# Kernel optimization log

Measured on AMD Instinct MI355X. Metric: run time of the kernel, lower is better.

## Reference

```python
import jax, jax.numpy as jnp
import numpy as np
from jax import lax

B, T, I, H = 8192, 512, 3, 25  # batch, seq_len, input_size, hidden_size


def setup_inputs() -> dict:
    key = jax.random.key(0)
    ks = jax.random.split(key, 4)
    x = jax.random.normal(ks[0], (B, T, I), dtype=jnp.float32)
    # xavier-uniform-ish scale for w_ih, orthogonal-ish (plain normal here) for w_hh
    w_ih = jax.random.normal(ks[1], (4 * H, I), dtype=jnp.float32) * 0.5
    w_hh = jax.random.normal(ks[2], (4 * H, H), dtype=jnp.float32) * 0.2
    b_ih = jnp.zeros((4 * H,), dtype=jnp.float32)
    # PyTorch init in module: forget-gate bias (second quarter) set to 1 on each bias
    b_ih = b_ih.at[H:2 * H].set(1.0)
    b_hh = jnp.zeros((4 * H,), dtype=jnp.float32)
    b_hh = b_hh.at[H:2 * H].set(1.0)
    w_lin = jax.random.normal(ks[3], (1, H), dtype=jnp.float32) * 0.3
    b_lin = jnp.zeros((1,), dtype=jnp.float32)
    return {"x": x, "w_ih": w_ih, "w_hh": w_hh, "b_ih": b_ih, "b_hh": b_hh,
            "w_lin": w_lin, "b_lin": b_lin}


def _lstm_last_h(x, w_ih, w_hh, b_ih, b_hh):
    # x: [B, T, I]; returns final hidden state h_T: [B, H]
    b = b_ih + b_hh  # [4H]
    xT = jnp.swapaxes(x, 0, 1)  # [T, B, I]

    def step(carry, x_t):
        h, c = carry
        gates = x_t @ w_ih.T + h @ w_hh.T + b  # [B, 4H]
        i, f, g, o = jnp.split(gates, 4, axis=-1)  # PyTorch gate order i,f,g,o
        i = jax.nn.sigmoid(i)
        f = jax.nn.sigmoid(f)
        g = jnp.tanh(g)
        o = jax.nn.sigmoid(o)
        c = f * c + i * g
        h = o * jnp.tanh(c)
        return (h, c), None

    h0 = jnp.zeros((x.shape[0], w_hh.shape[1]), dtype=x.dtype)
    (h, _), _ = lax.scan(step, (h0, h0), xT)
    return h


def reference(x, w_ih, w_hh, b_ih, b_hh, w_lin, b_lin):
    h_last = _lstm_last_h(x, w_ih, w_hh, b_ih, b_hh)  # [B, H]
    return h_last @ w_lin.T + b_lin  # [B, 1]
```

## Files before the change

kernel.cpp:

```cpp
#include <hip/hip_runtime.h>
#include <hip/hip_bf16.h>


#define TSTEPS 512
#define ISZ 3
#define HSZ 25
#define NW 7
#define CHUNK 256
#define TSTRIDE 40

typedef __attribute__((ext_vector_type(8))) short bf16x8;
typedef __attribute__((ext_vector_type(4))) float f32x4;

__device__ __forceinline__ unsigned short bf16_bits(float v) {
    return __builtin_bit_cast(unsigned short, __float2bfloat16(v));
}
__device__ __forceinline__ unsigned int pack_bf16(float lo, float hi) {
    return ((unsigned int)bf16_bits(hi) << 16) | (unsigned int)bf16_bits(lo);
}

__device__ __forceinline__ void lstm_act(const f32x4 acc, float& c, float& h) {
    const float K1 = 1.442695040888963f;
    const float K2 = 2.885390081777927f;
    const float e0 = __builtin_amdgcn_exp2f(-K1 * acc[0]);
    const float e1 = __builtin_amdgcn_exp2f(-K1 * acc[1]);
    const float e2 = __builtin_amdgcn_exp2f(fminf(-K2 * acc[2], 126.0f));
    const float e3 = __builtin_amdgcn_exp2f(-K1 * acc[3]);
    const float f  = __builtin_amdgcn_rcpf(1.0f + e1);
    const float ig = (1.0f - e2) * __builtin_amdgcn_rcpf((1.0f + e0) * (1.0f + e2));
    c = fmaf(f, c, ig);
    const float ec = __builtin_amdgcn_exp2f(fminf(-K2 * c, 126.0f));
    h = (1.0f - ec) * __builtin_amdgcn_rcpf((1.0f + e3) * (1.0f + ec));
}

__global__ __launch_bounds__(NW * 64) void lstm_mfma(
    const float* __restrict__ x,
    const float* __restrict__ w_ih,
    const float* __restrict__ w_hh,
    const float* __restrict__ b_ih,
    const float* __restrict__ b_hh,
    const float* __restrict__ w_lin,
    const float* __restrict__ b_lin,
    float* __restrict__ out)
{
    __shared__ uint2 xpk[2][CHUNK][16];
    __shared__ short hb[2][2][16 * TSTRIDE];
    __shared__ float outred[2][NW][16];

    const int tid  = threadIdx.x;
    const int w    = tid >> 6;
    const int lane = tid & 63;
    const int n    = lane & 15;
    const int q    = lane >> 4;
    const bool isq0 = (q == 0);
    const int u    = 4 * w + q;
    const bool act = (w < 6) || isq0;

    for (int i = tid; i < 2 * 2 * 16 * TSTRIDE; i += NW * 64) ((short*)hb)[i] = 0;

    auto stage = [&](int c0) {
        const int bsel = tid & 31;
        const int tile = bsel >> 4, nn = bsel & 15;
        const float* __restrict__ g =
            x + (size_t)(blockIdx.x * 32 + bsel) * (TSTEPS * ISZ) + c0 * ISZ;
        for (int tg = tid >> 5; tg < CHUNK / 4; tg += 14) {
            const float4* f4 = (const float4*)(g + tg * 12);
            float4 a = f4[0], b4 = f4[1], c4 = f4[2];
            const float s[4][3] = { {a.x, a.y, a.z}, {a.w, b4.x, b4.y},
                                    {b4.z, b4.w, c4.x}, {c4.y, c4.z, c4.w} };
            #pragma unroll
            for (int uu = 0; uu < 4; ++uu) {
                uint2 d;
                d.x = pack_bf16(s[uu][0], s[uu][1]);
                d.y = pack_bf16(s[uu][2], 1.0f);
                xpk[tile][tg * 4 + uu][nn] = d;
            }
        }
    };
    stage(0);

    bf16x8 afrag;
    #pragma unroll
    for (int j = 0; j < 8; ++j) {
        const int k = q * 8 + j;
        const int r = 16 * w + n;
        const int uu = r >> 2, g = r & 3;
        float v = 0.0f;
        if (uu < HSZ) {
            const int orow = g * HSZ + uu;
            if (k < ISZ)            v = w_ih[orow * ISZ + k];
            else if (k == ISZ)      v = b_ih[orow] + b_hh[orow];
            else if (k < 4 + HSZ)   v = w_hh[orow * HSZ + (k - 4)];
        }
        afrag[j] = (short)bf16_bits(v);
    }

    __syncthreads();

    float cA = 0.f, hA = 0.f, cB = 0.f, hB = 0.f;

    #pragma unroll 1
    for (int t = 0; t < TSTEPS; ++t) {
        if (t == CHUNK) {
            stage(CHUNK);
            __syncthreads();
        }
        const int ts = t & (CHUNK - 1);
        const uint2 xA = xpk[0][ts][n];
        const uint2 xB = xpk[1][ts][n];
        bf16x8 bfA = *reinterpret_cast<const bf16x8*>(&hb[t & 1][0][n * TSTRIDE + q * 8]);
        bf16x8 bfB = *reinterpret_cast<const bf16x8*>(&hb[t & 1][1][n * TSTRIDE + q * 8]);

        uint4 biA = __builtin_bit_cast(uint4, bfA);
        uint4 biB = __builtin_bit_cast(uint4, bfB);
        if (isq0) {
            biA.x = xA.x; biA.y = xA.y;
            biB.x = xB.x; biB.y = xB.y;
        }
        const f32x4 accA = __builtin_amdgcn_mfma_f32_16x16x32_bf16(
            afrag, __builtin_bit_cast(bf16x8, biA),
            (f32x4){0.f, 0.f, 0.f, 0.f}, 0, 0, 0);
        const f32x4 accB = __builtin_amdgcn_mfma_f32_16x16x32_bf16(
            afrag, __builtin_bit_cast(bf16x8, biB),
            (f32x4){0.f, 0.f, 0.f, 0.f}, 0, 0, 0);

        lstm_act(accA, cA, hA);
        lstm_act(accB, cB, hB);

        if (act) {
            hb[(t + 1) & 1][0][n * TSTRIDE + 4 + u] = (short)bf16_bits(hA);
            hb[(t + 1) & 1][1][n * TSTRIDE + 4 + u] = (short)bf16_bits(hB);
        }
        __syncthreads();
    }

    float vA = 0.f, vB = 0.f;
    if (act) { vA = w_lin[u] * hA; vB = w_lin[u] * hB; }
    vA += __shfl_xor(vA, 16); vA += __shfl_xor(vA, 32);
    vB += __shfl_xor(vB, 16); vB += __shfl_xor(vB, 32);
    if (lane < 16) { outred[0][w][lane] = vA; outred[1][w][lane] = vB; }
    __syncthreads();
    if (tid < 32) {
        const int tile = tid >> 4, nn = tid & 15;
        float s = b_lin[0];
        #pragma unroll
        for (int k = 0; k < NW; ++k) s += outred[tile][k][nn];
        out[blockIdx.x * 32 + tile * 16 + nn] = s;
    }
}

extern "C" void kernel_launch(void* const* d_in, const int* in_sizes, int n_in,
                              void* d_out, int out_size, void* d_ws, size_t ws_size,
                              hipStream_t stream) {
    const float* x     = (const float*)d_in[0];
    const float* w_ih  = (const float*)d_in[1];
    const float* w_hh  = (const float*)d_in[2];
    const float* b_ih  = (const float*)d_in[3];
    const float* b_hh  = (const float*)d_in[4];
    const float* w_lin = (const float*)d_in[5];
    const float* b_lin = (const float*)d_in[6];
    float* out = (float*)d_out;

    lstm_mfma<<<8192 / 32, NW * 64, 0, stream>>>(x, w_ih, w_hh, b_ih, b_hh,
                                                 w_lin, b_lin, out);
}
```

Baseline: 317.2 us.

## Shrink block to four waves, each computing two gate fragments per step

The block drops from seven waves to four. Each of the first three waves now computes two 16-row weight fragments per timestep (four MFMAs plus four activations), and the last wave handles the remaining fragment. The aim is to cut per-step barrier cost and increase work per wave, so the latency-bound recurrence spends less time synchronising. In exchange each wave's serial chain per step gets longer, the waves are imbalanced, and register use rises.

New measurement: 348.6 us. +9.9%, slower.

```diff
diff --git a/kernel.cpp b/kernel.cpp
--- a/kernel.cpp
+++ b/kernel.cpp
@@ -5,7 +5,7 @@
 #define TSTEPS 512
 #define ISZ 3
 #define HSZ 25
-#define NW 7
+#define NW 4
 #define CHUNK 256
 #define TSTRIDE 40
 
@@ -53,8 +53,13 @@
     const int n    = lane & 15;
     const int q    = lane >> 4;
     const bool isq0 = (q == 0);
-    const int u    = 4 * w + q;
-    const bool act = (w < 6) || isq0;
+
+    const int f0 = (w < 3) ? 2 * w : 6;
+    const int f1 = (w < 3) ? 2 * w + 1 : 6;
+    const bool use1 = (w < 3);
+    const int u0 = 4 * f0 + q;
+    const int u1 = 4 * f1 + q;
+    const bool m0 = (u0 < HSZ);
 
     for (int i = tid; i < 2 * 2 * 16 * TSTRIDE; i += NW * 64) ((short*)hb)[i] = 0;
 
@@ -63,7 +68,7 @@
         const int tile = bsel >> 4, nn = bsel & 15;
         const float* __restrict__ g =
             x + (size_t)(blockIdx.x * 32 + bsel) * (TSTEPS * ISZ) + c0 * ISZ;
-        for (int tg = tid >> 5; tg < CHUNK / 4; tg += 14) {
+        for (int tg = tid >> 5; tg < CHUNK / 4; tg += (NW * 64) / 32) {
             const float4* f4 = (const float4*)(g + tg * 12);
             float4 a = f4[0], b4 = f4[1], c4 = f4[2];
             const float s[4][3] = { {a.x, a.y, a.z}, {a.w, b4.x, b4.y},
@@ -79,25 +84,32 @@
     };
     stage(0);
 
-    bf16x8 afrag;
+    bf16x8 af0, af1;
     #pragma unroll
-    for (int j = 0; j < 8; ++j) {
-        const int k = q * 8 + j;
-        const int r = 16 * w + n;
-        const int uu = r >> 2, g = r & 3;
-        float v = 0.0f;
-        if (uu < HSZ) {
-            const int orow = g * HSZ + uu;
-            if (k < ISZ)            v = w_ih[orow * ISZ + k];
-            else if (k == ISZ)      v = b_ih[orow] + b_hh[orow];
-            else if (k < 4 + HSZ)   v = w_hh[orow * HSZ + (k - 4)];
-        }
-        afrag[j] = (short)bf16_bits(v);
+    for (int idx = 0; idx < 2; ++idx) {
+        const int T = idx ? f1 : f0;
+        bf16x8 af;
+        #pragma unroll
+        for (int j = 0; j < 8; ++j) {
+            const int k = q * 8 + j;
+            const int r = 16 * T + n;
+            const int uu = r >> 2, g = r & 3;
+            float v = 0.0f;
+            if (uu < HSZ) {
+                const int orow = g * HSZ + uu;
+                if (k < ISZ)            v = w_ih[orow * ISZ + k];
+                else if (k == ISZ)      v = b_ih[orow] + b_hh[orow];
+                else if (k < 4 + HSZ)   v = w_hh[orow * HSZ + (k - 4)];
+            }
+            af[j] = (short)bf16_bits(v);
+        }
+        if (idx) af1 = af; else af0 = af;
     }
 
     __syncthreads();
 
-    float cA = 0.f, hA = 0.f, cB = 0.f, hB = 0.f;
+    float c00 = 0.f, c01 = 0.f, c10 = 0.f, c11 = 0.f;
+    float h00 = 0.f, h01 = 0.f, h10 = 0.f, h11 = 0.f;
 
     #pragma unroll 1
     for (int t = 0; t < TSTEPS; ++t) {
@@ -117,25 +129,47 @@
             biA.x = xA.x; biA.y = xA.y;
             biB.x = xB.x; biB.y = xB.y;
         }
-        const f32x4 accA = __builtin_amdgcn_mfma_f32_16x16x32_bf16(
-            afrag, __builtin_bit_cast(bf16x8, biA),
-            (f32x4){0.f, 0.f, 0.f, 0.f}, 0, 0, 0);
-        const f32x4 accB = __builtin_amdgcn_mfma_f32_16x16x32_bf16(
-            afrag, __builtin_bit_cast(bf16x8, biB),
-            (f32x4){0.f, 0.f, 0.f, 0.f}, 0, 0, 0);
-
-        lstm_act(accA, cA, hA);
-        lstm_act(accB, cB, hB);
-
-        if (act) {
-            hb[(t + 1) & 1][0][n * TSTRIDE + 4 + u] = (short)bf16_bits(hA);
-            hb[(t + 1) & 1][1][n * TSTRIDE + 4 + u] = (short)bf16_bits(hB);
+        const bf16x8 bA = __builtin_bit_cast(bf16x8, biA);
+        const bf16x8 bB = __builtin_bit_cast(bf16x8, biB);
+
+        const f32x4 a00 = __builtin_amdgcn_mfma_f32_16x16x32_bf16(
+            af0, bA, (f32x4){0.f, 0.f, 0.f, 0.f}, 0, 0, 0);
+        const f32x4 a10 = __builtin_amdgcn_mfma_f32_16x16x32_bf16(
+            af0, bB, (f32x4){0.f, 0.f, 0.f, 0.f}, 0, 0, 0);
+        f32x4 a01, a11;
+        if (use1) {
+            a01 = __builtin_amdgcn_mfma_f32_16x16x32_bf16(
+                af1, bA, (f32x4){0.f, 0.f, 0.f, 0.f}, 0, 0, 0);
+            a11 = __builtin_amdgcn_mfma_f32_16x16x32_bf16(
+                af1, bB, (f32x4){0.f, 0.f, 0.f, 0.f}, 0, 0, 0);
+        }
+
+        lstm_act(a00, c00, h00);
+        lstm_act(a10, c10, h10);
+        if (use1) {
+            lstm_act(a01, c01, h01);
+            lstm_act(a11, c11, h11);
+        }
+
+        short* const wrA = &hb[(t + 1) & 1][0][n * TSTRIDE + 4];
+        short* const wrB = &hb[(t + 1) & 1][1][n * TSTRIDE + 4];
+        if (m0) {
+            wrA[u0] = (short)bf16_bits(h00);
+            wrB[u0] = (short)bf16_bits(h10);
+        }
+        if (use1) {
+            wrA[u1] = (short)bf16_bits(h01);
+            wrB[u1] = (short)bf16_bits(h11);
         }
         __syncthreads();
     }
 
     float vA = 0.f, vB = 0.f;
-    if (act) { vA = w_lin[u] * hA; vB = w_lin[u] * hB; }
+    if (m0) { vA = w_lin[u0] * h00; vB = w_lin[u0] * h10; }
+    if (use1) {
+        vA = fmaf(w_lin[u1], h01, vA);
+        vB = fmaf(w_lin[u1], h11, vB);
+    }
     vA += __shfl_xor(vA, 16); vA += __shfl_xor(vA, 32);
     vB += __shfl_xor(vB, 16); vB += __shfl_xor(vB, 32);
     if (lane < 16) { outred[0][w][lane] = vA; outred[1][w][lane] = vB; }
```
